# Optimization experiments

Hardware: AMD Instinct MI355X
Metric: run time of the kernel (lower is better)

The kernel has to match this reference:

```python
import jax, jax.numpy as jnp
import numpy as np

B, S, D, UNITS = 64, 2048, 512, 256

def setup_inputs() -> dict:
    key = jax.random.key(0)
    ks = jax.random.split(key, 8)
    sd = 1.0 / np.sqrt(D)
    query = jax.random.normal(ks[0], (B, D), dtype=jnp.float32)
    values = jax.random.normal(ks[1], (B, S, D), dtype=jnp.float32)
    W1 = jax.random.normal(ks[2], (D, UNITS), dtype=jnp.float32) * sd
    b1 = jnp.zeros((UNITS,), dtype=jnp.float32)
    W2 = jax.random.normal(ks[3], (D, UNITS), dtype=jnp.float32) * sd
    b2 = jnp.zeros((UNITS,), dtype=jnp.float32)
    V = jax.random.normal(ks[4], (UNITS, 1), dtype=jnp.float32) * (1.0 / np.sqrt(UNITS))
    bV = jnp.zeros((1,), dtype=jnp.float32)
    return {"query": query, "values": values, "W1": W1, "b1": b1,
            "W2": W2, "b2": b2, "V": V, "bV": bV}

def reference(query, values, W1, b1, W2, b2, V, bV):
    # proj_v: [B, S, U]; proj_q: [B, 1, U]
    proj_v = jnp.einsum('bsd,du->bsu', values, W1) + b1
    proj_q = (query @ W2 + b2)[:, None, :]
    # score: [B, S, 1]
    score = jnp.tanh(proj_v + proj_q) @ V + bV
    attn = jax.nn.softmax(score, axis=1)           # softmax over sequence axis
    context = jnp.sum(attn * values, axis=1)        # [B, D]
    return context
```

## Files before the change

kernel.cpp:

```cpp
#include <hip/hip_runtime.h>
#include <hip/hip_bf16.h>

typedef unsigned short u16;
typedef unsigned int u32;
typedef __attribute__((ext_vector_type(8))) short short8;
typedef __attribute__((ext_vector_type(4))) float f32x4;

#define NB 64
#define NS 2048
#define ND 512
#define NU 256
#define CH 64
#define CPB (NS / CH)
#define ASTR 520

__device__ __forceinline__ u16 f2b(float f) {
    u32 x = __float_as_uint(f);
    u32 r = (x + 0x7FFFu + ((x >> 16) & 1u)) >> 16;
    return (u16)r;
}
__device__ __forceinline__ u32 pk2(float lo, float hi) {
    __hip_bfloat162 h = __float22bfloat162_rn(float2{lo, hi});
    return *(u32*)&h;
}
__device__ __forceinline__ float fast_tanh(float x) {
    float e = __expf(2.0f * x);
    return 1.0f - 2.0f / (e + 1.0f);
}

__global__ __launch_bounds__(256) void prep_kernel(
    const float* __restrict__ q, const float* __restrict__ W2,
    const float* __restrict__ b1, const float* __restrict__ b2,
    const float* __restrict__ W1,
    float* __restrict__ cb, u16* __restrict__ W1Tf)
{
    const int tid = threadIdx.x;
    if (blockIdx.x < 64) {
        int b = blockIdx.x, u = tid;
        __shared__ float qs[ND];
        qs[u]       = q[b * ND + u];
        qs[u + 256] = q[b * ND + u + 256];
        __syncthreads();
        float acc = 0.f;
#pragma unroll 8
        for (int d = 0; d < ND; d++)
            acc += qs[d] * W2[d * NU + u];
        cb[b * NU + u] = acc + b1[u] + b2[u];
    } else {
        int blk = blockIdx.x - 64;
#pragma unroll
        for (int it = 0; it < 8; it++) {
            int id   = blk * 2048 + it * 256 + tid;
            int f    = id >> 6, lane = id & 63;
            int cbk  = f & 3, kh = (f >> 2) & 1, wn = (f >> 3) & 3, kc = f >> 5;
            int m16  = lane & 15, quad = lane >> 4;
            int u    = wn * 64 + cbk * 16 + m16;
            int kb   = kc * 64 + kh * 32 + quad * 8;
            u16 tmp[8];
#pragma unroll
            for (int j = 0; j < 8; j++)
                tmp[j] = f2b(W1[(kb + j) * NU + u]);
            *(uint4*)&W1Tf[(size_t)id * 8] = *(uint4*)tmp;
        }
    }
}

__global__ __launch_bounds__(256, 2) void fused_kernel(
    const float* __restrict__ values,
    const u16* __restrict__ W1Tf,
    const float* __restrict__ cb,
    const float* __restrict__ V,
    float* __restrict__ ctxp,
    float2* __restrict__ meta)
{
    const int tid  = threadIdx.x;
    const int lane = tid & 63;
    const int wn   = tid >> 6;
    const int m16  = lane & 15;
    const int quad = lane >> 4;

    const int mblk = blockIdx.x;
    const int b    = mblk >> 5;
    const size_t base_row = (size_t)mblk * CH;

    __shared__ u16 Afull[CH][ASTR];
    __shared__ float cbs[NU];
    __shared__ float Vs[NU];
    __shared__ float rsum4[4][CH];
    __shared__ float wsm[CH];
    __shared__ float mred[2];

    cbs[tid] = cb[b * NU + tid];
    Vs[tid]  = V[tid];

    const int arow = tid >> 2;
    const int acol = (tid & 3) * 16;
    const float* asrc = values + (base_row + arow) * ND + (tid & 3) * 16;
#pragma unroll
    for (int h = 0; h < 2; h++) {
        float4 v[4][4];
#pragma unroll
        for (int k4 = 0; k4 < 4; k4++)
#pragma unroll
            for (int j = 0; j < 4; j++)
                v[k4][j] = ((const float4*)(asrc + (h * 4 + k4) * 64))[j];
#pragma unroll
        for (int k4 = 0; k4 < 4; k4++) {
            int kc = h * 4 + k4;
            uint4 q0, q1;
            q0.x = pk2(v[k4][0].x, v[k4][0].y); q0.y = pk2(v[k4][0].z, v[k4][0].w);
            q0.z = pk2(v[k4][1].x, v[k4][1].y); q0.w = pk2(v[k4][1].z, v[k4][1].w);
            q1.x = pk2(v[k4][2].x, v[k4][2].y); q1.y = pk2(v[k4][2].z, v[k4][2].w);
            q1.z = pk2(v[k4][3].x, v[k4][3].y); q1.w = pk2(v[k4][3].z, v[k4][3].w);
            *(uint4*)&Afull[arow][kc * 64 + acol]     = q0;
            *(uint4*)&Afull[arow][kc * 64 + acol + 8] = q1;
        }
    }
    __syncthreads();

    f32x4 acc[4][4] = {};
    const u16* pB = W1Tf + wn * 4096 + lane * 8;

    short8 bfr[2][8];
#pragma unroll
    for (int f = 0; f < 8; f++)
        bfr[0][f] = *(const short8*)(pB + f * 512);

#pragma unroll
    for (int kc = 0; kc < 8; kc++) {
        const int cur = kc & 1, nxt = cur ^ 1;
        if (kc < 7) {
#pragma unroll
            for (int f = 0; f < 8; f++)
                bfr[nxt][f] = *(const short8*)(pB + (kc + 1) * 16384 + f * 512);
        }
        short8 afr[2][4];
#pragma unroll
        for (int kh = 0; kh < 2; kh++)
#pragma unroll
            for (int rb = 0; rb < 4; rb++)
                afr[kh][rb] = *(const short8*)&Afull[rb * 16 + m16][kc * 64 + kh * 32 + quad * 8];
#pragma unroll
        for (int kh = 0; kh < 2; kh++)
#pragma unroll
            for (int rb = 0; rb < 4; rb++)
#pragma unroll
                for (int cbk = 0; cbk < 4; cbk++)
                    acc[rb][cbk] = __builtin_amdgcn_mfma_f32_16x16x32_bf16(
                        afr[kh][rb], bfr[cur][kh * 4 + cbk], acc[rb][cbk], 0, 0, 0);
    }

    float cbv[4], vv[4];
#pragma unroll
    for (int cbk = 0; cbk < 4; cbk++) {
        int c = wn * 64 + cbk * 16 + m16;
        cbv[cbk] = cbs[c];
        vv[cbk]  = Vs[c];
    }
#pragma unroll
    for (int rb = 0; rb < 4; rb++) {
#pragma unroll
        for (int i = 0; i < 4; i++) {
            float s = 0.f;
#pragma unroll
            for (int cbk = 0; cbk < 4; cbk++)
                s += fast_tanh(acc[rb][cbk][i] + cbv[cbk]) * vv[cbk];
            s += __shfl_xor(s, 1, 64);
            s += __shfl_xor(s, 2, 64);
            s += __shfl_xor(s, 4, 64);
            s += __shfl_xor(s, 8, 64);
            if (m16 == 0)
                rsum4[wn][rb * 16 + quad * 4 + i] = s;
        }
    }
    __syncthreads();

    if (tid < CH) {
        float s = rsum4[0][tid] + rsum4[1][tid] + rsum4[2][tid] + rsum4[3][tid];
        float m = s;
        m = fmaxf(m, __shfl_xor(m, 1, 64));
        m = fmaxf(m, __shfl_xor(m, 2, 64));
        m = fmaxf(m, __shfl_xor(m, 4, 64));
        m = fmaxf(m, __shfl_xor(m, 8, 64));
        m = fmaxf(m, __shfl_xor(m, 16, 64));
        m = fmaxf(m, __shfl_xor(m, 32, 64));
        float w = __expf(s - m);
        wsm[tid] = w;
        float l = w;
        l += __shfl_xor(l, 1, 64);
        l += __shfl_xor(l, 2, 64);
        l += __shfl_xor(l, 4, 64);
        l += __shfl_xor(l, 8, 64);
        l += __shfl_xor(l, 16, 64);
        l += __shfl_xor(l, 32, 64);
        if (tid == 0) { mred[0] = m; mred[1] = l; }
    }
    __syncthreads();

    {
        const u32* adw = (const u32*)&Afull[0][0];
        float a0 = 0.f, a1 = 0.f;
#pragma unroll 8
        for (int r = 0; r < CH; r++) {
            u32 pk = adw[r * (ASTR / 2) + tid];
            float lo = __uint_as_float(pk << 16);
            float hi = __uint_as_float(pk & 0xFFFF0000u);
            float wt = wsm[r];
            a0 += wt * lo;
            a1 += wt * hi;
        }
        float2* dst = (float2*)(ctxp + (size_t)mblk * ND + tid * 2);
        *dst = float2{a0, a1};
    }
    if (tid == 0) meta[mblk] = float2{mred[0], mred[1]};
}

__global__ __launch_bounds__(256) void combine_kernel(
    const float* __restrict__ ctxp, const float2* __restrict__ meta,
    float* __restrict__ out)
{
    int b = blockIdx.x, tid = threadIdx.x;
    __shared__ float wc[CPB];
    __shared__ float Ls;
    if (tid < CPB) {
        float2 mt = meta[b * CPB + tid];
        float m = mt.x;
        m = fmaxf(m, __shfl_xor(m, 1, 64));
        m = fmaxf(m, __shfl_xor(m, 2, 64));
        m = fmaxf(m, __shfl_xor(m, 4, 64));
        m = fmaxf(m, __shfl_xor(m, 8, 64));
        m = fmaxf(m, __shfl_xor(m, 16, 64));
        float w = __expf(mt.x - m);
        wc[tid] = w;
        float l = w * mt.y;
        l += __shfl_xor(l, 1, 64);
        l += __shfl_xor(l, 2, 64);
        l += __shfl_xor(l, 4, 64);
        l += __shfl_xor(l, 8, 64);
        l += __shfl_xor(l, 16, 64);
        if (tid == 0) Ls = l;
    }
    __syncthreads();
    float inv = 1.0f / Ls;
    float s0 = 0.f, s1 = 0.f;
#pragma unroll 4
    for (int c = 0; c < CPB; c++) {
        const float* p = ctxp + ((size_t)b * CPB + c) * ND;
        float w = wc[c];
        s0 += w * p[tid];
        s1 += w * p[tid + 256];
    }
    out[b * ND + tid]       = s0 * inv;
    out[b * ND + tid + 256] = s1 * inv;
}

extern "C" void kernel_launch(void* const* d_in, const int* in_sizes, int n_in,
                              void* d_out, int out_size, void* d_ws, size_t ws_size,
                              hipStream_t stream)
{
    const float* q      = (const float*)d_in[0];
    const float* values = (const float*)d_in[1];
    const float* W1     = (const float*)d_in[2];
    const float* b1     = (const float*)d_in[3];
    const float* W2     = (const float*)d_in[4];
    const float* b2     = (const float*)d_in[5];
    const float* V      = (const float*)d_in[6];

    char* ws = (char*)d_ws;
    float*  cb    = (float*) (ws);
    u16*    W1Tf  = (u16*)   (ws + 65536);
    float*  ctxp  = (float*) (ws + 327680);
    float2* meta  = (float2*)(ws + 327680 + 4194304);

    hipLaunchKernelGGL(prep_kernel, dim3(72), dim3(256), 0, stream,
                       q, W2, b1, b2, W1, cb, W1Tf);
    hipLaunchKernelGGL(fused_kernel, dim3(NB * CPB), dim3(256), 0, stream,
                       values, W1Tf, cb, V, ctxp, meta);
    hipLaunchKernelGGL(combine_kernel, dim3(64), dim3(256), 0, stream,
                       ctxp, meta, (float*)d_out);
}
```

Baseline: 445.4 us.

## Loop each block over eight 32-row chunks with double-buffered LDS prefetch

The fused kernel now runs 512 blocks. Each block walks eight consecutive 32-row chunks instead of handling a single 64-row chunk. While one chunk's MFMA, tanh-score and context work runs, the fp32 values for the next chunk are loaded into registers, then converted to bf16 into the alternate LDS buffer. The goal is to hide global-load latency behind compute. The cost is that W1 fragments are reloaded once per 32 rows, so B operands get half the reuse. The number of partial chunks doubles, so combine_kernel now reduces 64 partials per batch and the workspace layout is resized.

```diff
diff --git a/kernel.cpp b/kernel.cpp
--- a/kernel.cpp
+++ b/kernel.cpp
@@ -10,8 +10,10 @@
 #define NS 2048
 #define ND 512
 #define NU 256
-#define CH 64
+#define CH 32
 #define CPB (NS / CH)
+#define CHBLK 8
+#define GRID (NB * CPB / CHBLK)
 #define ASTR 520
 
 __device__ __forceinline__ u16 f2b(float f) {
@@ -26,6 +28,10 @@
 __device__ __forceinline__ float fast_tanh(float x) {
     float e = __expf(2.0f * x);
     return 1.0f - 2.0f / (e + 1.0f);
+}
+__device__ __forceinline__ void wg_barrier() {
+    asm volatile("s_waitcnt lgkmcnt(0)" ::: "memory");
+    __builtin_amdgcn_s_barrier();
 }
 
 __global__ __launch_bounds__(256) void prep_kernel(
@@ -79,140 +85,164 @@
     const int m16  = lane & 15;
     const int quad = lane >> 4;
 
-    const int mblk = blockIdx.x;
-    const int b    = mblk >> 5;
-    const size_t base_row = (size_t)mblk * CH;
-
-    __shared__ u16 Afull[CH][ASTR];
+    const int chunk0 = blockIdx.x * CHBLK;
+    const int b      = chunk0 >> 6;
+
+    __shared__ u16 Abuf[2][CH][ASTR];
     __shared__ float cbs[NU];
     __shared__ float Vs[NU];
     __shared__ float rsum4[4][CH];
     __shared__ float wsm[CH];
-    __shared__ float mred[2];
 
     cbs[tid] = cb[b * NU + tid];
     Vs[tid]  = V[tid];
 
-    const int arow = tid >> 2;
-    const int acol = (tid & 3) * 16;
-    const float* asrc = values + (base_row + arow) * ND + (tid & 3) * 16;
-#pragma unroll
-    for (int h = 0; h < 2; h++) {
-        float4 v[4][4];
-#pragma unroll
-        for (int k4 = 0; k4 < 4; k4++)
+    const int r  = tid >> 3;
+    const int k8 = tid & 7;
+    const float* abase = values + ((size_t)chunk0 * CH + r) * ND + k8 * 16;
+
+    const u16* pB = W1Tf + wn * 4096 + lane * 8;
+
+    {
+        float4 av[4][4];
+#pragma unroll
+        for (int j = 0; j < 4; j++)
+#pragma unroll
+            for (int qq = 0; qq < 4; qq++)
+                av[j][qq] = ((const float4*)(abase + j * 128))[qq];
+#pragma unroll
+        for (int j = 0; j < 4; j++) {
+            uint4 q0, q1;
+            q0.x = pk2(av[j][0].x, av[j][0].y); q0.y = pk2(av[j][0].z, av[j][0].w);
+            q0.z = pk2(av[j][1].x, av[j][1].y); q0.w = pk2(av[j][1].z, av[j][1].w);
+            q1.x = pk2(av[j][2].x, av[j][2].y); q1.y = pk2(av[j][2].z, av[j][2].w);
+            q1.z = pk2(av[j][3].x, av[j][3].y); q1.w = pk2(av[j][3].z, av[j][3].w);
+            *(uint4*)&Abuf[0][r][k8 * 16 + j * 128]     = q0;
+            *(uint4*)&Abuf[0][r][k8 * 16 + j * 128 + 8] = q1;
+        }
+    }
+    wg_barrier();
+
+    for (int c = 0; c < CHBLK; c++) {
+        const int p = c & 1;
+        const int chunk = chunk0 + c;
+
+        float4 av[4][4];
+        if (c < CHBLK - 1) {
+            const float* src = abase + (size_t)(c + 1) * CH * ND;
 #pragma unroll
             for (int j = 0; j < 4; j++)
-                v[k4][j] = ((const float4*)(asrc + (h * 4 + k4) * 64))[j];
-#pragma unroll
-        for (int k4 = 0; k4 < 4; k4++) {
-            int kc = h * 4 + k4;
-            uint4 q0, q1;
-            q0.x = pk2(v[k4][0].x, v[k4][0].y); q0.y = pk2(v[k4][0].z, v[k4][0].w);
-            q0.z = pk2(v[k4][1].x, v[k4][1].y); q0.w = pk2(v[k4][1].z, v[k4][1].w);
-            q1.x = pk2(v[k4][2].x, v[k4][2].y); q1.y = pk2(v[k4][2].z, v[k4][2].w);
-            q1.z = pk2(v[k4][3].x, v[k4][3].y); q1.w = pk2(v[k4][3].z, v[k4][3].w);
-            *(uint4*)&Afull[arow][kc * 64 + acol]     = q0;
-            *(uint4*)&Afull[arow][kc * 64 + acol + 8] = q1;
-        }
-    }
-    __syncthreads();
-
-    f32x4 acc[4][4] = {};
-    const u16* pB = W1Tf + wn * 4096 + lane * 8;
-
-    short8 bfr[2][8];
-#pragma unroll
-    for (int f = 0; f < 8; f++)
-        bfr[0][f] = *(const short8*)(pB + f * 512);
-
-#pragma unroll
-    for (int kc = 0; kc < 8; kc++) {
-        const int cur = kc & 1, nxt = cur ^ 1;
-        if (kc < 7) {
-#pragma unroll
-            for (int f = 0; f < 8; f++)
-                bfr[nxt][f] = *(const short8*)(pB + (kc + 1) * 16384 + f * 512);
-        }
-        short8 afr[2][4];
-#pragma unroll
-        for (int kh = 0; kh < 2; kh++)
-#pragma unroll
-            for (int rb = 0; rb < 4; rb++)
-                afr[kh][rb] = *(const short8*)&Afull[rb * 16 + m16][kc * 64 + kh * 32 + quad * 8];
-#pragma unroll
-        for (int kh = 0; kh < 2; kh++)
-#pragma unroll
-            for (int rb = 0; rb < 4; rb++)
-#pragma unroll
-                for (int cbk = 0; cbk < 4; cbk++)
-                    acc[rb][cbk] = __builtin_amdgcn_mfma_f32_16x16x32_bf16(
-                        afr[kh][rb], bfr[cur][kh * 4 + cbk], acc[rb][cbk], 0, 0, 0);
-    }
-
-    float cbv[4], vv[4];
-#pragma unroll
-    for (int cbk = 0; cbk < 4; cbk++) {
-        int c = wn * 64 + cbk * 16 + m16;
-        cbv[cbk] = cbs[c];
-        vv[cbk]  = Vs[c];
-    }
-#pragma unroll
-    for (int rb = 0; rb < 4; rb++) {
-#pragma unroll
-        for (int i = 0; i < 4; i++) {
-            float s = 0.f;
-#pragma unroll
-            for (int cbk = 0; cbk < 4; cbk++)
-                s += fast_tanh(acc[rb][cbk][i] + cbv[cbk]) * vv[cbk];
-            s += __shfl_xor(s, 1, 64);
-            s += __shfl_xor(s, 2, 64);
-            s += __shfl_xor(s, 4, 64);
-            s += __shfl_xor(s, 8, 64);
-            if (m16 == 0)
-                rsum4[wn][rb * 16 + quad * 4 + i] = s;
-        }
-    }
-    __syncthreads();
-
-    if (tid < CH) {
-        float s = rsum4[0][tid] + rsum4[1][tid] + rsum4[2][tid] + rsum4[3][tid];
-        float m = s;
-        m = fmaxf(m, __shfl_xor(m, 1, 64));
-        m = fmaxf(m, __shfl_xor(m, 2, 64));
-        m = fmaxf(m, __shfl_xor(m, 4, 64));
-        m = fmaxf(m, __shfl_xor(m, 8, 64));
-        m = fmaxf(m, __shfl_xor(m, 16, 64));
-        m = fmaxf(m, __shfl_xor(m, 32, 64));
-        float w = __expf(s - m);
-        wsm[tid] = w;
-        float l = w;
-        l += __shfl_xor(l, 1, 64);
-        l += __shfl_xor(l, 2, 64);
-        l += __shfl_xor(l, 4, 64);
-        l += __shfl_xor(l, 8, 64);
-        l += __shfl_xor(l, 16, 64);
-        l += __shfl_xor(l, 32, 64);
-        if (tid == 0) { mred[0] = m; mred[1] = l; }
-    }
-    __syncthreads();
-
-    {
-        const u32* adw = (const u32*)&Afull[0][0];
-        float a0 = 0.f, a1 = 0.f;
+#pragma unroll
+                for (int qq = 0; qq < 4; qq++)
+                    av[j][qq] = ((const float4*)(src + j * 128))[qq];
+        }
+
+        f32x4 acc[2][4] = {};
+        short8 bfr[2][8];
+#pragma unroll
+        for (int f = 0; f < 8; f++)
+            bfr[0][f] = *(const short8*)(pB + f * 512);
+#pragma unroll
+        for (int kc = 0; kc < 8; kc++) {
+            const int cur = kc & 1;
+            if (kc < 7) {
+#pragma unroll
+                for (int f = 0; f < 8; f++)
+                    bfr[cur ^ 1][f] = *(const short8*)(pB + (kc + 1) * 16384 + f * 512);
+            }
+            short8 afr[2][2];
+#pragma unroll
+            for (int kh = 0; kh < 2; kh++)
+#pragma unroll
+                for (int rb = 0; rb < 2; rb++)
+                    afr[kh][rb] = *(const short8*)&Abuf[p][rb * 16 + m16][kc * 64 + kh * 32 + quad * 8];
+#pragma unroll
+            for (int kh = 0; kh < 2; kh++)
+#pragma unroll
+                for (int rb = 0; rb < 2; rb++)
+#pragma unroll
+                    for (int cbk = 0; cbk < 4; cbk++)
+                        acc[rb][cbk] = __builtin_amdgcn_mfma_f32_16x16x32_bf16(
+                            afr[kh][rb], bfr[cur][kh * 4 + cbk], acc[rb][cbk], 0, 0, 0);
+        }
+
+        {
+            float cbv[4], vv[4];
+#pragma unroll
+            for (int cbk = 0; cbk < 4; cbk++) {
+                int cc = wn * 64 + cbk * 16 + m16;
+                cbv[cbk] = cbs[cc];
+                vv[cbk]  = Vs[cc];
+            }
+#pragma unroll
+            for (int rb = 0; rb < 2; rb++) {
+#pragma unroll
+                for (int i = 0; i < 4; i++) {
+                    float s = 0.f;
+#pragma unroll
+                    for (int cbk = 0; cbk < 4; cbk++)
+                        s += fast_tanh(acc[rb][cbk][i] + cbv[cbk]) * vv[cbk];
+                    s += __shfl_xor(s, 1, 64);
+                    s += __shfl_xor(s, 2, 64);
+                    s += __shfl_xor(s, 4, 64);
+                    s += __shfl_xor(s, 8, 64);
+                    if (m16 == 0)
+                        rsum4[wn][rb * 16 + quad * 4 + i] = s;
+                }
+            }
+        }
+        wg_barrier();
+
+        if (tid < CH) {
+            float s = rsum4[0][tid] + rsum4[1][tid] + rsum4[2][tid] + rsum4[3][tid];
+            float m = s;
+            m = fmaxf(m, __shfl_xor(m, 1, 64));
+            m = fmaxf(m, __shfl_xor(m, 2, 64));
+            m = fmaxf(m, __shfl_xor(m, 4, 64));
+            m = fmaxf(m, __shfl_xor(m, 8, 64));
+            m = fmaxf(m, __shfl_xor(m, 16, 64));
+            float w = __expf(s - m);
+            wsm[tid] = w;
+            float l = w;
+            l += __shfl_xor(l, 1, 64);
+            l += __shfl_xor(l, 2, 64);
+            l += __shfl_xor(l, 4, 64);
+            l += __shfl_xor(l, 8, 64);
+            l += __shfl_xor(l, 16, 64);
+            if (tid == 0) meta[chunk] = float2{m, l};
+        }
+        wg_barrier();
+
+        {
+            const u32* adw = (const u32*)&Abuf[p][0][0];
+            float a0 = 0.f, a1 = 0.f;
 #pragma unroll 8
-        for (int r = 0; r < CH; r++) {
-            u32 pk = adw[r * (ASTR / 2) + tid];
-            float lo = __uint_as_float(pk << 16);
-            float hi = __uint_as_float(pk & 0xFFFF0000u);
-            float wt = wsm[r];
-            a0 += wt * lo;
-            a1 += wt * hi;
-        }
-        float2* dst = (float2*)(ctxp + (size_t)mblk * ND + tid * 2);
-        *dst = float2{a0, a1};
-    }
-    if (tid == 0) meta[mblk] = float2{mred[0], mred[1]};
+            for (int rr = 0; rr < CH; rr++) {
+                u32 pk = adw[rr * (ASTR / 2) + tid];
+                float lo = __uint_as_float(pk << 16);
+                float hi = __uint_as_float(pk & 0xFFFF0000u);
+                float wt = wsm[rr];
+                a0 += wt * lo;
+                a1 += wt * hi;
+            }
+            float2* dst = (float2*)(ctxp + (size_t)chunk * ND + tid * 2);
+            *dst = float2{a0, a1};
+        }
+
+        if (c < CHBLK - 1) {
+#pragma unroll
+            for (int j = 0; j < 4; j++) {
+                uint4 q0, q1;
+                q0.x = pk2(av[j][0].x, av[j][0].y); q0.y = pk2(av[j][0].z, av[j][0].w);
+                q0.z = pk2(av[j][1].x, av[j][1].y); q0.w = pk2(av[j][1].z, av[j][1].w);
+                q1.x = pk2(av[j][2].x, av[j][2].y); q1.y = pk2(av[j][2].z, av[j][2].w);
+                q1.z = pk2(av[j][3].x, av[j][3].y); q1.w = pk2(av[j][3].z, av[j][3].w);
+                *(uint4*)&Abuf[p ^ 1][r][k8 * 16 + j * 128]     = q0;
+                *(uint4*)&Abuf[p ^ 1][r][k8 * 16 + j * 128 + 8] = q1;
+            }
+            wg_barrier();
+        }
+    }
 }
 
 __global__ __launch_bounds__(256) void combine_kernel(
@@ -230,6 +260,7 @@
         m = fmaxf(m, __shfl_xor(m, 4, 64));
         m = fmaxf(m, __shfl_xor(m, 8, 64));
         m = fmaxf(m, __shfl_xor(m, 16, 64));
+        m = fmaxf(m, __shfl_xor(m, 32, 64));
         float w = __expf(mt.x - m);
         wc[tid] = w;
         float l = w * mt.y;
@@ -238,6 +269,7 @@
         l += __shfl_xor(l, 4, 64);
         l += __shfl_xor(l, 8, 64);
         l += __shfl_xor(l, 16, 64);
+        l += __shfl_xor(l, 32, 64);
         if (tid == 0) Ls = l;
     }
     __syncthreads();
@@ -270,11 +302,11 @@
     float*  cb    = (float*) (ws);
     u16*    W1Tf  = (u16*)   (ws + 65536);
     float*  ctxp  = (float*) (ws + 327680);
-    float2* meta  = (float2*)(ws + 327680 + 4194304);
+    float2* meta  = (float2*)(ws + 327680 + 8388608);
 
     hipLaunchKernelGGL(prep_kernel, dim3(72), dim3(256), 0, stream,
                        q, W2, b1, b2, W1, cb, W1Tf);
-    hipLaunchKernelGGL(fused_kernel, dim3(NB * CPB), dim3(256), 0, stream,
+    hipLaunchKernelGGL(fused_kernel, dim3(GRID), dim3(256), 0, stream,
                        values, W1Tf, cb, V, ctxp, meta);
     hipLaunchKernelGGL(combine_kernel, dim3(64), dim3(256), 0, stream,
                        ctxp, meta, (float*)d_out);
```

Result: slower. 535.6 us (+20.3%).
